# Kernel optimization log

Measured on AMD Instinct MI355X. Metric: run time of the kernel, lower is better.

## Reference

```python
import jax, jax.numpy as jnp
import numpy as np

N_NODES = 100000
N_EDGES = 3200000
D_FEAT = 128
HIDDEN = 16
N_CLASSES = 7


def gcn_conv(x, edge_index, edge_weight, W, b, n_nodes):
    h = x @ W  # dense projection first (Fout small)
    src, dst = edge_index[0], edge_index[1]
    # add self-loops with weight 1
    loop = jnp.arange(n_nodes, dtype=edge_index.dtype)
    src_a = jnp.concatenate([src, loop])
    dst_a = jnp.concatenate([dst, loop])
    ew_a = jnp.concatenate([edge_weight, jnp.ones((n_nodes,), dtype=x.dtype)])
    deg = jax.ops.segment_sum(ew_a, dst_a, num_segments=n_nodes)
    dinv = jnp.where(deg > 0, jax.lax.rsqrt(deg), 0.0)
    norm = dinv[src_a] * ew_a * dinv[dst_a]  # [E+N]
    msg = h[src_a] * norm[:, None]  # gather + scale
    out = jax.ops.segment_sum(msg, dst_a, num_segments=n_nodes)
    return out + b


def setup_inputs() -> dict:
    key = jax.random.key(0)
    k = jax.random.split(key, 8)
    x = jax.random.normal(k[0], (N_NODES, D_FEAT), dtype=jnp.float32)
    edge_index = jax.random.randint(k[1], (2, N_EDGES), 0, N_NODES, dtype=jnp.int64)
    edge_weight = jax.random.uniform(k[2], (N_EDGES,), dtype=jnp.float32)
    s1 = 1.0 / np.sqrt(D_FEAT)
    s2 = 1.0 / np.sqrt(HIDDEN)
    W1 = jax.random.uniform(k[3], (D_FEAT, HIDDEN), jnp.float32, -s1, s1)
    b1 = jnp.zeros((HIDDEN,), jnp.float32)
    W2 = jax.random.uniform(k[4], (HIDDEN, N_CLASSES), jnp.float32, -s2, s2)
    b2 = jnp.zeros((N_CLASSES,), jnp.float32)
    return {"x": x, "edge_index": edge_index, "edge_weight": edge_weight,
            "W1": W1, "b1": b1, "W2": W2, "b2": b2}


def reference(x, edge_index, edge_weight, W1, b1, W2, b2):
    h = jax.nn.relu(gcn_conv(x, edge_index, edge_weight, W1, b1, N_NODES))
    out = gcn_conv(h, edge_index, edge_weight, W2, b2, N_NODES)
    return jax.nn.log_softmax(out, axis=1)
```

## Files before the change

kernel.cpp:

```cpp
#include <hip/hip_runtime.h>
#include <hip/hip_fp16.h>
#include <math.h>

constexpr int NN = 100000;
constexpr int NE = 3200000;
constexpr int DF = 128;
constexpr int NH = 16;
constexpr int NC = 7;

constexpr int BN    = 128;
constexpr int NB    = (NN + BN - 1) / BN;
constexpr int CAP   = 4608;
constexpr int CHUNK = 8192;
constexpr int AB    = (NE + CHUNK - 1) / CHUNK;
constexpr int EPT   = CHUNK / 1024;
constexpr int SPT   = (CAP + 1023) / 1024;

constexpr float QS   = 32767.0f;
constexpr float QINV = 1.0f / 32767.0f;

__global__ void k_zero(int* __restrict__ gcur) {
    int t = blockIdx.x * blockDim.x + threadIdx.x;
    if (t < NB) gcur[t] = 0;
}

__global__ void __launch_bounds__(1024)
k_append(const int* __restrict__ src,
         const int* __restrict__ dst,
         const float* __restrict__ w,
         int* __restrict__ gcur,
         uint2* __restrict__ ebuf) {
    __shared__ int hist[NB];
    __shared__ int basev[NB];
    for (int i = threadIdx.x; i < NB; i += 1024) hist[i] = 0;
    __syncthreads();
    int e0 = blockIdx.x * CHUNK;
    unsigned slo[EPT], sw[EPT];
    int sbr[EPT];
#pragma unroll
    for (int k = 0; k < EPT; ++k) {
        int e = e0 + (int)threadIdx.x + k * 1024;
        sbr[k] = -1;
        if (e < NE) {
            int d = __builtin_nontemporal_load(dst + e);
            int b = d >> 7;
            int r = atomicAdd(&hist[b], 1);
            slo[k] = ((unsigned)(d & (BN - 1)) << 17) |
                     (unsigned)__builtin_nontemporal_load(src + e);
            sw[k]  = __float_as_uint(__builtin_nontemporal_load(w + e));
            sbr[k] = (b << 14) | r;
        }
    }
    __syncthreads();
    for (int b = threadIdx.x; b < NB; b += 1024) {
        int c = hist[b];
        basev[b] = (c > 0) ? atomicAdd(&gcur[b], c) : 0;
    }
    __syncthreads();
#pragma unroll
    for (int k = 0; k < EPT; ++k) {
        if (sbr[k] >= 0) {
            int b = sbr[k] >> 14;
            int pos = basev[b] + (sbr[k] & 0x3FFF);
            if (pos < CAP) {
                uint2 v; v.x = slo[k]; v.y = sw[k];
                ebuf[(size_t)b * CAP + pos] = v;
            }
        }
    }
}

__global__ void __launch_bounds__(1024)
k_sort(const int* __restrict__ gcur,
       uint2* __restrict__ ebuf,
       int* __restrict__ rs,
       int* __restrict__ rc,
       float* __restrict__ dinv) {
    __shared__ int cursor[BN];
    __shared__ int scanS[BN];
    __shared__ int startEx[BN];
    __shared__ unsigned sorted[CAP];
    int b = blockIdx.x;
    int tid = threadIdx.x;
    int cnt = min(gcur[b], CAP);
    const uint2* eb = ebuf + (size_t)b * CAP;
    if (tid < BN) cursor[tid] = 0;
    __syncthreads();
    unsigned sval[SPT];
    int sdr[SPT];
#pragma unroll
    for (int k = 0; k < SPT; ++k) {
        int i = tid + k * 1024;
        sdr[k] = -1;
        if (i < cnt) {
            uint2 v = eb[i];
            int dl = (v.x >> 17) & (BN - 1);
            unsigned q = (unsigned)(__uint_as_float(v.y) * QS + 0.5f);
            int r = atomicAdd(&cursor[dl], 1);
            sval[k] = (v.x & 0x1FFFF) | (q << 17);
            sdr[k] = (dl << 13) | r;
        }
    }
    __syncthreads();
    if (tid < BN) scanS[tid] = cursor[tid];
    __syncthreads();
    for (int off = 1; off < BN; off <<= 1) {
        int v = (tid < BN && tid >= off) ? scanS[tid - off] : 0;
        __syncthreads();
        if (tid < BN) scanS[tid] += v;
        __syncthreads();
    }
    if (tid < BN) {
        int ex = scanS[tid] - cursor[tid];
        startEx[tid] = ex;
        int n = b * BN + tid;
        if (n < NN) { rs[n] = b * CAP * 2 + ex; rc[n] = cursor[tid]; }
    }
    __syncthreads();
#pragma unroll
    for (int k = 0; k < SPT; ++k) {
        if (sdr[k] >= 0)
            sorted[startEx[sdr[k] >> 13] + (sdr[k] & 0x1FFF)] = sval[k];
    }
    __syncthreads();
    unsigned* eb32 = (unsigned*)ebuf + (size_t)b * CAP * 2;
    for (int i = tid; i < cnt; i += 1024) eb32[i] = sorted[i];
    if (tid < BN) {
        int n = b * BN + tid;
        if (n < NN) {
            float s = 1.0f;
            int s0 = startEx[tid], c = cursor[tid];
            for (int i = 0; i < c; ++i) s += (float)(sorted[s0 + i] >> 17) * QINV;
            dinv[n] = rsqrtf(s);
        }
    }
}

__global__ void k_proj1(const float* __restrict__ x,
                        const float* __restrict__ W1,
                        const float* __restrict__ dinv,
                        __half* __restrict__ h1p) {
    __shared__ float Ws[DF * NH];
    for (int i = threadIdx.x; i < DF * NH; i += blockDim.x) Ws[i] = W1[i];
    __syncthreads();
    int t = blockIdx.x * blockDim.x + threadIdx.x;
    if (t >= NN * NH) return;
    int n = t >> 4;
    int f = t & 15;
    const float4* xr = (const float4*)(x + (size_t)n * DF);
    float acc = 0.0f;
#pragma unroll
    for (int k4 = 0; k4 < DF / 4; ++k4) {
        float4 xv = xr[k4];
        acc += xv.x * Ws[(k4 * 4 + 0) * NH + f];
        acc += xv.y * Ws[(k4 * 4 + 1) * NH + f];
        acc += xv.z * Ws[(k4 * 4 + 2) * NH + f];
        acc += xv.w * Ws[(k4 * 4 + 3) * NH + f];
    }
    h1p[t] = __float2half(acc * dinv[n]);
}

__global__ void __launch_bounds__(1024)
k_agg1(const int* __restrict__ rs,
       const int* __restrict__ rc,
       const unsigned* __restrict__ cbuf,
       const __half* __restrict__ h1p,
       float* __restrict__ acc1) {
    const __half2* hp = (const __half2*)h1p;
    int t = blockIdx.x * 1024 + threadIdx.x;
    int n = t >> 3;
    int f2 = t & 7;
    if (n >= NN) return;
    float2 g0 = __half22float2(hp[n * 8 + f2]);
    float ax = g0.x, ay = g0.y;
    int s0 = rs[n], c = rc[n];
    int i = 0;
    for (; i + 1 < c; i += 2) {
        unsigned e0 = cbuf[s0 + i];
        unsigned e1 = cbuf[s0 + i + 1];
        float2 v0 = __half22float2(hp[(e0 & 0x1FFFF) * 8 + f2]);
        float2 v1 = __half22float2(hp[(e1 & 0x1FFFF) * 8 + f2]);
        float w0 = (float)(e0 >> 17) * QINV;
        float w1 = (float)(e1 >> 17) * QINV;
        ax += w0 * v0.x + w1 * v1.x;
        ay += w0 * v0.y + w1 * v1.y;
    }
    if (i < c) {
        unsigned e0 = cbuf[s0 + i];
        float2 v0 = __half22float2(hp[(e0 & 0x1FFFF) * 8 + f2]);
        float w0 = (float)(e0 >> 17) * QINV;
        ax += w0 * v0.x;
        ay += w0 * v0.y;
    }
    float2 r; r.x = ax; r.y = ay;
    ((float2*)acc1)[n * 8 + f2] = r;
}

__global__ void k_relu_proj2(const float* __restrict__ acc1,
                             const float* __restrict__ dinv,
                             const float* __restrict__ b1,
                             const float* __restrict__ W2,
                             __half* __restrict__ h2p) {
    int n = blockIdx.x * blockDim.x + threadIdx.x;
    if (n >= NN) return;
    float di = dinv[n];
    float hr[NH];
#pragma unroll
    for (int k = 0; k < NH; ++k)
        hr[k] = fmaxf(di * acc1[n * NH + k] + b1[k], 0.0f);
#pragma unroll
    for (int c = 0; c < NC; ++c) {
        float a = 0.0f;
#pragma unroll
        for (int k = 0; k < NH; ++k) a += hr[k] * W2[k * NC + c];
        h2p[n * 8 + c] = __float2half(di * a);
    }
    h2p[n * 8 + 7] = __float2half(0.0f);
}

__global__ void __launch_bounds__(1024)
k_agg2_lsm(const int* __restrict__ rs,
           const int* __restrict__ rc,
           const unsigned* __restrict__ cbuf,
           const __half* __restrict__ h2p,
           const float* __restrict__ dinv,
           const float* __restrict__ b2,
           float* __restrict__ out) {
    const __half2* hp = (const __half2*)h2p;
    int t = blockIdx.x * 1024 + threadIdx.x;
    int n = t >> 2;
    int c2 = t & 3;
    if (n >= NN) return;
    float2 g0 = __half22float2(hp[n * 4 + c2]);
    float ax = g0.x, ay = g0.y;
    int s0 = rs[n], c = rc[n];
    int i = 0;
    for (; i + 1 < c; i += 2) {
        unsigned e0 = cbuf[s0 + i];
        unsigned e1 = cbuf[s0 + i + 1];
        float2 v0 = __half22float2(hp[(e0 & 0x1FFFF) * 4 + c2]);
        float2 v1 = __half22float2(hp[(e1 & 0x1FFFF) * 4 + c2]);
        float w0 = (float)(e0 >> 17) * QINV;
        float w1 = (float)(e1 >> 17) * QINV;
        ax += w0 * v0.x + w1 * v1.x;
        ay += w0 * v0.y + w1 * v1.y;
    }
    if (i < c) {
        unsigned e0 = cbuf[s0 + i];
        float2 v0 = __half22float2(hp[(e0 & 0x1FFFF) * 4 + c2]);
        float w0 = (float)(e0 >> 17) * QINV;
        ax += w0 * v0.x;
        ay += w0 * v0.y;
    }
    float di = dinv[n];
    float va = di * ax + b2[2 * c2];
    float vb = (c2 < 3) ? (di * ay + b2[2 * c2 + 1]) : -1e30f;
    float m = fmaxf(va, vb);
#pragma unroll
    for (int mask = 1; mask < 4; mask <<= 1)
        m = fmaxf(m, __shfl_xor(m, mask, 4));
    float s = __expf(va - m) + ((c2 < 3) ? __expf(vb - m) : 0.0f);
#pragma unroll
    for (int mask = 1; mask < 4; mask <<= 1)
        s += __shfl_xor(s, mask, 4);
    float lse = m + __logf(s);
    out[n * NC + 2 * c2] = va - lse;
    if (c2 < 3) out[n * NC + 2 * c2 + 1] = vb - lse;
}

extern "C" void kernel_launch(void* const* d_in, const int* in_sizes, int n_in,
                              void* d_out, int out_size, void* d_ws, size_t ws_size,
                              hipStream_t stream) {
    const float* x  = (const float*)d_in[0];
    const int*   ei = (const int*)d_in[1];
    const float* ew = (const float*)d_in[2];
    const float* W1 = (const float*)d_in[3];
    const float* b1 = (const float*)d_in[4];
    const float* W2 = (const float*)d_in[5];
    const float* b2 = (const float*)d_in[6];
    float* out = (float*)d_out;

    const int* srcp = ei;
    const int* dstp = ei + NE;

    float*  ws   = (float*)d_ws;
    float*  dinv = ws;
    __half* h1p  = (__half*)(ws + 100352);
    float*  acc1 = ws + 900352;
    int*    gcur = (int*)(ws + 2500352);
    int*    rs   = (int*)(ws + 2501376);
    int*    rc   = (int*)(ws + 2601728);
    uint2*  ebuf = (uint2*)(ws + 2702080);
    const unsigned* cbuf = (const unsigned*)ebuf;
    __half* h2p  = h1p;

    const int B = 256;
    auto cdiv = [](long long a, long long b) { return (int)((a + b - 1) / b); };

    k_zero<<<1, 1024, 0, stream>>>(gcur);
    k_append<<<AB, 1024, 0, stream>>>(srcp, dstp, ew, gcur, ebuf);
    k_sort<<<NB, 1024, 0, stream>>>(gcur, ebuf, rs, rc, dinv);
    k_proj1<<<cdiv((long long)NN * NH, B), B, 0, stream>>>(x, W1, dinv, h1p);
    k_agg1<<<cdiv((long long)NN * 8, 1024), 1024, 0, stream>>>(rs, rc, cbuf, h1p, acc1);
    k_relu_proj2<<<cdiv(NN, B), B, 0, stream>>>(acc1, dinv, b1, W2, h2p);
    k_agg2_lsm<<<cdiv((long long)NN * 4, 1024), 1024, 0, stream>>>(rs, rc, cbuf, h2p, dinv, b2, out);
}
```

Before: 259.4 us.

## Register-tile layer-1 projection and fuse ReLU/projection-2 into aggregation

The first projection now has each thread compute four full 16-wide output rows, reading W1 as float4 from shared memory. Before, 16 threads each reread the same x row and produced one output. The relu/W2 projection is folded into the first aggregation kernel through an 8-lane shuffle reduction. This removes the fp32 acc1 round trip and one launch. The trade-off is more registers per thread in the projection and extra shuffle work in the aggregation. Each thread's four x rows sit 512 bytes apart, so those loads may coalesce less well.

Result: slower. 265.8 us (+2.5%).

```diff
diff --git a/kernel.cpp b/kernel.cpp
--- a/kernel.cpp
+++ b/kernel.cpp
@@ -136,36 +136,77 @@
     }
 }
 
-__global__ void k_proj1(const float* __restrict__ x,
-                        const float* __restrict__ W1,
-                        const float* __restrict__ dinv,
-                        __half* __restrict__ h1p) {
-    __shared__ float Ws[DF * NH];
-    for (int i = threadIdx.x; i < DF * NH; i += blockDim.x) Ws[i] = W1[i];
-    __syncthreads();
-    int t = blockIdx.x * blockDim.x + threadIdx.x;
-    if (t >= NN * NH) return;
-    int n = t >> 4;
-    int f = t & 15;
-    const float4* xr = (const float4*)(x + (size_t)n * DF);
-    float acc = 0.0f;
-#pragma unroll
+__global__ void __launch_bounds__(256)
+k_proj1(const float* __restrict__ x,
+        const float* __restrict__ W1,
+        const float* __restrict__ dinv,
+        __half* __restrict__ h1p) {
+    __shared__ float4 Ws[DF * 4];
+    {
+        const float4* w4 = (const float4*)W1;
+        for (int i = threadIdx.x; i < DF * 4; i += 256) Ws[i] = w4[i];
+    }
+    __syncthreads();
+    int base = (blockIdx.x * 256 + threadIdx.x) * 4;
+    if (base >= NN) return;
+    float4 acc[4][4];
+#pragma unroll
+    for (int j = 0; j < 4; ++j)
+#pragma unroll
+        for (int q = 0; q < 4; ++q) acc[j][q] = make_float4(0.f, 0.f, 0.f, 0.f);
+    int nv = min(4, NN - base);
+    const float4* xr0 = (const float4*)(x + (size_t)base * DF);
+#pragma unroll 4
     for (int k4 = 0; k4 < DF / 4; ++k4) {
-        float4 xv = xr[k4];
-        acc += xv.x * Ws[(k4 * 4 + 0) * NH + f];
-        acc += xv.y * Ws[(k4 * 4 + 1) * NH + f];
-        acc += xv.z * Ws[(k4 * 4 + 2) * NH + f];
-        acc += xv.w * Ws[(k4 * 4 + 3) * NH + f];
-    }
-    h1p[t] = __float2half(acc * dinv[n]);
+        float4 xv[4];
+#pragma unroll
+        for (int j = 0; j < 4; ++j)
+            xv[j] = (j < nv) ? xr0[(size_t)j * 32 + k4] : make_float4(0.f, 0.f, 0.f, 0.f);
+#pragma unroll
+        for (int kk = 0; kk < 4; ++kk) {
+            float4 w0 = Ws[(k4 * 4 + kk) * 4 + 0];
+            float4 w1 = Ws[(k4 * 4 + kk) * 4 + 1];
+            float4 w2 = Ws[(k4 * 4 + kk) * 4 + 2];
+            float4 w3 = Ws[(k4 * 4 + kk) * 4 + 3];
+#pragma unroll
+            for (int j = 0; j < 4; ++j) {
+                float xs = (kk == 0) ? xv[j].x : (kk == 1) ? xv[j].y : (kk == 2) ? xv[j].z : xv[j].w;
+                acc[j][0].x += xs * w0.x; acc[j][0].y += xs * w0.y;
+                acc[j][0].z += xs * w0.z; acc[j][0].w += xs * w0.w;
+                acc[j][1].x += xs * w1.x; acc[j][1].y += xs * w1.y;
+                acc[j][1].z += xs * w1.z; acc[j][1].w += xs * w1.w;
+                acc[j][2].x += xs * w2.x; acc[j][2].y += xs * w2.y;
+                acc[j][2].z += xs * w2.z; acc[j][2].w += xs * w2.w;
+                acc[j][3].x += xs * w3.x; acc[j][3].y += xs * w3.y;
+                acc[j][3].z += xs * w3.z; acc[j][3].w += xs * w3.w;
+            }
+        }
+    }
+    __half2* hp = (__half2*)h1p;
+#pragma unroll
+    for (int j = 0; j < 4; ++j) {
+        if (j >= nv) break;
+        int n = base + j;
+        float di = dinv[n];
+#pragma unroll
+        for (int q = 0; q < 4; ++q) {
+            float2 lo; lo.x = acc[j][q].x * di; lo.y = acc[j][q].y * di;
+            float2 hi; hi.x = acc[j][q].z * di; hi.y = acc[j][q].w * di;
+            hp[n * 8 + 2 * q]     = __float22half2_rn(lo);
+            hp[n * 8 + 2 * q + 1] = __float22half2_rn(hi);
+        }
+    }
 }
 
 __global__ void __launch_bounds__(1024)
-k_agg1(const int* __restrict__ rs,
-       const int* __restrict__ rc,
-       const unsigned* __restrict__ cbuf,
-       const __half* __restrict__ h1p,
-       float* __restrict__ acc1) {
+k_agg1p(const int* __restrict__ rs,
+        const int* __restrict__ rc,
+        const unsigned* __restrict__ cbuf,
+        const __half* __restrict__ h1p,
+        const float* __restrict__ dinv,
+        const float* __restrict__ b1,
+        const float* __restrict__ W2,
+        __half* __restrict__ h2p) {
     const __half2* hp = (const __half2*)h1p;
     int t = blockIdx.x * 1024 + threadIdx.x;
     int n = t >> 3;
@@ -192,30 +233,24 @@
         ax += w0 * v0.x;
         ay += w0 * v0.y;
     }
-    float2 r; r.x = ax; r.y = ay;
-    ((float2*)acc1)[n * 8 + f2] = r;
-}
-
-__global__ void k_relu_proj2(const float* __restrict__ acc1,
-                             const float* __restrict__ dinv,
-                             const float* __restrict__ b1,
-                             const float* __restrict__ W2,
-                             __half* __restrict__ h2p) {
-    int n = blockIdx.x * blockDim.x + threadIdx.x;
-    if (n >= NN) return;
     float di = dinv[n];
-    float hr[NH];
-#pragma unroll
-    for (int k = 0; k < NH; ++k)
-        hr[k] = fmaxf(di * acc1[n * NH + k] + b1[k], 0.0f);
-#pragma unroll
-    for (int c = 0; c < NC; ++c) {
-        float a = 0.0f;
-#pragma unroll
-        for (int k = 0; k < NH; ++k) a += hr[k] * W2[k * NC + c];
-        h2p[n * 8 + c] = __float2half(di * a);
-    }
-    h2p[n * 8 + 7] = __float2half(0.0f);
+    float hr0 = fmaxf(di * ax + b1[2 * f2], 0.0f);
+    float hr1 = fmaxf(di * ay + b1[2 * f2 + 1], 0.0f);
+    float p[NC];
+#pragma unroll
+    for (int cc = 0; cc < NC; ++cc)
+        p[cc] = hr0 * W2[(2 * f2) * NC + cc] + hr1 * W2[(2 * f2 + 1) * NC + cc];
+#pragma unroll
+    for (int mask = 1; mask < 8; mask <<= 1) {
+#pragma unroll
+        for (int cc = 0; cc < NC; ++cc)
+            p[cc] += __shfl_xor(p[cc], mask, 8);
+    }
+    float tv = 0.0f;
+#pragma unroll
+    for (int cc = 0; cc < NC; ++cc)
+        if (f2 == cc) tv = p[cc];
+    h2p[n * 8 + f2] = __float2half(di * tv);
 }
 
 __global__ void __launch_bounds__(1024)
@@ -286,22 +321,19 @@
     float*  ws   = (float*)d_ws;
     float*  dinv = ws;
     __half* h1p  = (__half*)(ws + 100352);
-    float*  acc1 = ws + 900352;
-    int*    gcur = (int*)(ws + 2500352);
-    int*    rs   = (int*)(ws + 2501376);
-    int*    rc   = (int*)(ws + 2601728);
-    uint2*  ebuf = (uint2*)(ws + 2702080);
+    __half* h2p  = (__half*)(ws + 900352);
+    int*    gcur = (int*)(ws + 1300352);
+    int*    rs   = (int*)(ws + 1301376);
+    int*    rc   = (int*)(ws + 1401728);
+    uint2*  ebuf = (uint2*)(ws + 1502080);
     const unsigned* cbuf = (const unsigned*)ebuf;
-    __half* h2p  = h1p;
-
-    const int B = 256;
+
     auto cdiv = [](long long a, long long b) { return (int)((a + b - 1) / b); };
 
     k_zero<<<1, 1024, 0, stream>>>(gcur);
     k_append<<<AB, 1024, 0, stream>>>(srcp, dstp, ew, gcur, ebuf);
     k_sort<<<NB, 1024, 0, stream>>>(gcur, ebuf, rs, rc, dinv);
-    k_proj1<<<cdiv((long long)NN * NH, B), B, 0, stream>>>(x, W1, dinv, h1p);
-    k_agg1<<<cdiv((long long)NN * 8, 1024), 1024, 0, stream>>>(rs, rc, cbuf, h1p, acc1);
-    k_relu_proj2<<<cdiv(NN, B), B, 0, stream>>>(acc1, dinv, b1, W2, h2p);
+    k_proj1<<<cdiv(NN, 1024), 256, 0, stream>>>(x, W1, dinv, h1p);
+    k_agg1p<<<cdiv((long long)NN * 8, 1024), 1024, 0, stream>>>(rs, rc, cbuf, h1p, dinv, b1, W2, h2p);
     k_agg2_lsm<<<cdiv((long long)NN * 4, 1024), 1024, 0, stream>>>(rs, rc, cbuf, h2p, dinv, b2, out);
 }
```
